# Optimization experiments

Measured on AMD Instinct MI355X. Metric: run time of the kernel, lower is better.

The kernel has to match this reference:

```python
import jax, jax.numpy as jnp
import numpy as np

H1, H2, IN, LAT = 64, 32, 2, 16

def _lstm(x, Wih, Whh, bih, bhh, H):
    # x: [B, T, I]; gate order i,f,g,o (PyTorch convention)
    B, T, _ = x.shape
    xg = jnp.einsum('bti,gi->btg', x, Wih) + bih + bhh  # [B, T, 4H]
    xg = jnp.transpose(xg, (1, 0, 2))  # [T, B, 4H]

    def step(carry, xg_t):
        h, c = carry
        gates = xg_t + h @ Whh.T
        i, f, g, o = jnp.split(gates, 4, axis=-1)
        i = jax.nn.sigmoid(i); f = jax.nn.sigmoid(f)
        g = jnp.tanh(g); o = jax.nn.sigmoid(o)
        c = f * c + i * g
        h = o * jnp.tanh(c)
        return (h, c), h

    h0 = jnp.zeros((B, H), x.dtype)
    c0 = jnp.zeros((B, H), x.dtype)
    (h_last, _), hs = jax.lax.scan(step, (h0, c0), xg)
    return jnp.transpose(hs, (1, 0, 2)), h_last  # [B,T,H], [B,H]


def setup_inputs() -> dict:
    key = jax.random.key(0)
    ks = jax.random.split(key, 12)
    s = 0.1
    return {
        'x': jax.random.normal(ks[0], (512, 4096, IN), jnp.float32),
        'Wih1': jax.random.normal(ks[1], (4 * H1, IN), jnp.float32) * s,
        'Whh1': jax.random.normal(ks[2], (4 * H1, H1), jnp.float32) * s,
        'bih1': jax.random.normal(ks[3], (4 * H1,), jnp.float32) * s,
        'bhh1': jax.random.normal(ks[4], (4 * H1,), jnp.float32) * s,
        'Wih2': jax.random.normal(ks[5], (4 * H2, H1), jnp.float32) * s,
        'Whh2': jax.random.normal(ks[6], (4 * H2, H2), jnp.float32) * s,
        'bih2': jax.random.normal(ks[7], (4 * H2,), jnp.float32) * s,
        'bhh2': jax.random.normal(ks[8], (4 * H2,), jnp.float32) * s,
        'Wfc': jax.random.normal(ks[9], (LAT, H2), jnp.float32) * s,
        'bfc': jax.random.normal(ks[10], (LAT,), jnp.float32) * s,
    }


def reference(x, Wih1, Whh1, bih1, bhh1, Wih2, Whh2, bih2, bhh2, Wfc, bfc):
    h1_seq, _ = _lstm(x, Wih1, Whh1, bih1, bhh1, H1)      # [B,T,64]
    _, h2_last = _lstm(h1_seq, Wih2, Whh2, bih2, bhh2, H2)  # [B,32] == x[:, -1, :]
    return h2_last @ Wfc.T + bfc  # [B,16]
```

## Files before the change

kernel.cpp:

```cpp
#include <hip/hip_runtime.h>


#define TT 4096
#define BB 512
#define NCH 64

typedef float    f4  __attribute__((ext_vector_type(4)));
typedef int      i4  __attribute__((ext_vector_type(4)));
typedef _Float16 h2v __attribute__((ext_vector_type(2)));
typedef _Float16 h8  __attribute__((ext_vector_type(8)));

__device__ __forceinline__ float fexp2(float x){ return __builtin_amdgcn_exp2f(x); }
__device__ __forceinline__ float frcp (float x){ return __builtin_amdgcn_rcpf(x); }
__device__ __forceinline__ float lgs  (float p){ return frcp(1.0f + fexp2(p)); }
__device__ __forceinline__ float tanh_(float x){ return 1.0f - 2.0f * frcp(1.0f + fexp2(x * 2.8853900817779268f)); }

#define BARRIER() asm volatile("s_waitcnt lgkmcnt(0)\n\ts_barrier" ::: "memory")

template<int CTRL>
__device__ __forceinline__ float qperm(float v){
  const int s = __builtin_bit_cast(int, v);
  return __builtin_bit_cast(float, __builtin_amdgcn_update_dpp(s, s, CTRL, 0xF, 0xF, true));
}
__device__ __forceinline__ h2v bch(int s){ return __builtin_bit_cast(h2v, s); }
__device__ __forceinline__ float dot8(h8 a, i4 bi, float c){
  const i4 ai = __builtin_bit_cast(i4, a);
  c = __builtin_amdgcn_fdot2(bch(ai.x), bch(bi.x), c, false);
  c = __builtin_amdgcn_fdot2(bch(ai.y), bch(bi.y), c, false);
  c = __builtin_amdgcn_fdot2(bch(ai.z), bch(bi.z), c, false);
  c = __builtin_amdgcn_fdot2(bch(ai.w), bch(bi.w), c, false);
  return c;
}
__device__ __forceinline__ float fdh(int a, int b, float c){
  return __builtin_amdgcn_fdot2(bch(a), bch(b), c, false);
}
__device__ __forceinline__ int pack16(float a, float b){
  h2v p; p.x = (_Float16)a; p.y = (_Float16)b;
  return __builtin_bit_cast(int, p);
}
__device__ __forceinline__ h8 ldh8s(const float* p, float s){
  const f4 a = ((const f4*)p)[0], b = ((const f4*)p)[1];
  h8 r;
  r[0]=(_Float16)(a.x*s); r[1]=(_Float16)(a.y*s); r[2]=(_Float16)(a.z*s); r[3]=(_Float16)(a.w*s);
  r[4]=(_Float16)(b.x*s); r[5]=(_Float16)(b.y*s); r[6]=(_Float16)(b.z*s); r[7]=(_Float16)(b.w*s);
  return r;
}

extern "C" __global__ __launch_bounds__(256, 1) void lstm_enc_kernel(
    const float* __restrict__ x,
    const float* __restrict__ Wih1, const float* __restrict__ Whh1,
    const float* __restrict__ bih1, const float* __restrict__ bhh1,
    const float* __restrict__ Wih2, const float* __restrict__ Whh2,
    const float* __restrict__ bih2, const float* __restrict__ bhh2,
    const float* __restrict__ Wfc,  const float* __restrict__ bfc,
    float* __restrict__ out)
{
    const int tid = threadIdx.x;
    const int l   = tid & 63;
    const int wv  = __builtin_amdgcn_readfirstlane(tid >> 6);
    const int be  = wv >> 1;
    const bool isL1 = ((wv & 1) == 0);
    const int bg  = blockIdx.x * 2 + be;

    __shared__ __align__(16) _Float16 ring[2][128][64];
    __shared__ __align__(16) _Float16 h2r[2][2][32];
    __shared__ int xs[2][2][64];

    const float kSs = -1.4426950408889634f;
    const float kSg = -2.8853900817779268f;

    if (isL1) {
        h8 wi[8], wf[8], wg[8], wo[8];
        const int ri = l, rf = 64 + l, rg = 128 + l, ro = 192 + l;
        #pragma unroll
        for (int j = 0; j < 8; ++j) {
            wi[j] = ldh8s(Whh1 + ri*64 + j*8, kSs);
            wf[j] = ldh8s(Whh1 + rf*64 + j*8, kSs);
            wg[j] = ldh8s(Whh1 + rg*64 + j*8, kSg);
            wo[j] = ldh8s(Whh1 + ro*64 + j*8, kSs);
        }
        const int wxi = pack16(Wih1[ri*2]*kSs, Wih1[ri*2+1]*kSs);
        const int wxf = pack16(Wih1[rf*2]*kSs, Wih1[rf*2+1]*kSs);
        const int wxg = pack16(Wih1[rg*2]*kSg, Wih1[rg*2+1]*kSg);
        const int wxo = pack16(Wih1[ro*2]*kSs, Wih1[ro*2+1]*kSs);
        const float bi_ = (bih1[ri] + bhh1[ri]) * kSs;
        const float bf_ = (bih1[rf] + bhh1[rf]) * kSs;
        const float bg_ = (bih1[rg] + bhh1[rg]) * kSg;
        const float bo_ = (bih1[ro] + bhh1[ro]) * kSs;

        if (l < 32) ((int*)&ring[be][127][0])[l] = 0;
        BARRIER();

        float cc = 0.f;
        _Float16* rw = &ring[be][0][0];
        const i4* rd = (const i4*)&ring[be][0][0];

#define L1S(PR, CR, XV) { \
    const i4* Hp = rd + (PR)*8; \
    i4 H[8]; \
    _Pragma("unroll") for (int j = 0; j < 8; ++j) H[j] = Hp[j]; \
    float ai = bi_, af = bf_, ag = bg_, ao = bo_; \
    _Pragma("unroll") for (int j = 0; j < 8; ++j) { \
        ai = dot8(wi[j], H[j], ai); af = dot8(wf[j], H[j], af); \
        ag = dot8(wg[j], H[j], ag); ao = dot8(wo[j], H[j], ao); } \
    const int xv_ = (XV); \
    ai = fdh(wxi, xv_, ai); af = fdh(wxf, xv_, af); \
    ag = fdh(wxg, xv_, ag); ao = fdh(wxo, xv_, ao); \
    const float gi = lgs(ai), gf = lgs(af), go = lgs(ao); \
    const float gg = fmaf(2.f, lgs(ag), -1.f); \
    cc = fmaf(gf, cc, gi * gg); \
    rw[(CR)*64 + l] = (_Float16)(go * tanh_(cc)); }

        #pragma unroll 1
        for (int c = 0; c <= NCH; ++c) {
            if (c < NCH) {
                const int base = (c & 1) * 64;
                const int p0 = (base ^ 64) + 63;
                const int* xc = xs[be][c & 1];
                L1S(p0, base, xc[0])
                #pragma unroll 2
                for (int s = 1; s < 64; ++s) { L1S(base + s - 1, base + s, xc[s]) }
            }
            BARRIER();
        }
#undef L1S
    } else {
        const int u = l & 31, hf = l >> 5;
        const float hff = (float)hf;
        const int rA = hf * 64 + u;
        const int rB = hf * 64 + 32 + u;
        const float kA = hf ? kSg : kSs;
        h8 wa[12], wb[12];
        #pragma unroll
        for (int j = 0; j < 8; ++j) {
            wa[j] = ldh8s(Wih2 + rA*64 + j*8, kA);
            wb[j] = ldh8s(Wih2 + rB*64 + j*8, kSs);
        }
        #pragma unroll
        for (int j = 0; j < 4; ++j) {
            wa[8+j] = ldh8s(Whh2 + rA*32 + j*8, kA);
            wb[8+j] = ldh8s(Whh2 + rB*32 + j*8, kSs);
        }
        const float ba_ = (bih2[rA] + bhh2[rA]) * kA;
        const float bb_ = (bih2[rB] + bhh2[rB]) * kSs;

        const float2* xb2 = (const float2*)(x + (size_t)bg * (TT * 2));
        {
            const float2 c0 = xb2[l];
            xs[be][0][l] = pack16(c0.x, c0.y);
        }
        float2 vxn = xb2[64 + l];
        BARRIER();

        float c2 = 0.f;
        int hp2 = 0;
        const i4* rdh = (const i4*)&ring[be][0][0];
        _Float16* q0 = &h2r[be][0][0];
        _Float16* q1 = &h2r[be][1][0];

#define L2S(S, QW) { \
    const i4* Hp = rc + (S)*8; \
    i4 H[8]; \
    _Pragma("unroll") for (int j = 0; j < 8; ++j) H[j] = Hp[j]; \
    i4 G[4]; \
    _Pragma("unroll") for (int j = 0; j < 4; ++j) { \
        G[j].x = __builtin_amdgcn_readlane(hp2, j*8+0); \
        G[j].y = __builtin_amdgcn_readlane(hp2, j*8+2); \
        G[j].z = __builtin_amdgcn_readlane(hp2, j*8+4); \
        G[j].w = __builtin_amdgcn_readlane(hp2, j*8+6); } \
    float pa = ba_, pb = bb_; \
    _Pragma("unroll") for (int j = 0; j < 8; ++j) { \
        pa = dot8(wa[j], H[j], pa); pb = dot8(wb[j], H[j], pb); } \
    _Pragma("unroll") for (int j = 0; j < 4; ++j) { \
        pa = dot8(wa[8+j], G[j], pa); pb = dot8(wb[8+j], G[j], pb); } \
    const float sa = lgs(pa); \
    const float va = fmaf(hff, sa - 1.f, sa);    \
    const float vb = lgs(pb);                    \
    const float oa = __shfl_xor(va, 32); \
    const float ob = __shfl_xor(vb, 32); \
    const float gi = hf ? oa : va, gf = hf ? ob : vb; \
    const float gg = hf ? va : oa, go = hf ? vb : ob; \
    c2 = fmaf(gf, c2, gi * gg); \
    const float h2n = go * tanh_(c2); \
    hp2 = pack16(h2n, qperm<0xB1>(h2n)); \
    if (!hf) (QW)[u] = (_Float16)h2n; }

        #pragma unroll 1
        for (int c = 0; c <= NCH; ++c) {
            if (c + 1 < NCH) xs[be][(c + 1) & 1][l] = pack16(vxn.x, vxn.y);
            if (c + 2 < NCH) vxn = xb2[(c + 2) * 64 + l];
            if (c > 0) {
                const i4* rc = rdh + ((c - 1) & 1) * 64 * 8;
                for (int s = 0; s < 64; s += 2) {
                    L2S(s,     q0)
                    L2S(s + 1, q1)
                }
            }
            BARRIER();
        }
#undef L2S

        if (l < 16) {
            float sum = bfc[l];
            const float* wr = Wfc + l * 32;
            #pragma unroll
            for (int k = 0; k < 32; ++k) sum = fmaf(wr[k], (float)h2r[be][1][k], sum);
            out[bg * 16 + l] = sum;
        }
    }
}

extern "C" void kernel_launch(void* const* d_in, const int* in_sizes, int n_in,
                              void* d_out, int out_size, void* d_ws, size_t ws_size,
                              hipStream_t stream) {
    const float* x    = (const float*)d_in[0];
    const float* Wih1 = (const float*)d_in[1];
    const float* Whh1 = (const float*)d_in[2];
    const float* bih1 = (const float*)d_in[3];
    const float* bhh1 = (const float*)d_in[4];
    const float* Wih2 = (const float*)d_in[5];
    const float* Whh2 = (const float*)d_in[6];
    const float* bih2 = (const float*)d_in[7];
    const float* bhh2 = (const float*)d_in[8];
    const float* Wfc  = (const float*)d_in[9];
    const float* bfc  = (const float*)d_in[10];

    hipLaunchKernelGGL(lstm_enc_kernel, dim3(BB / 2), dim3(256), 0, stream,
        x, Wih1, Whh1, bih1, bhh1, Wih2, Whh2, bih2, bhh2, Wfc, bfc,
        (float*)d_out);
}
```

Baseline: 1.557 ms.

## Feed x to layer-1 via readlane and double-buffer layer-2 ring reads

Layer-1 waves now load their own x chunk from global memory into a register and pass each timestep's value with readlane. This replaces the shared-memory xs buffer that the layer-2 waves used to fill, and removes the per-step LDS read of x on the layer-1 critical path. Layer-2 software-pipelines its ring reads: the h1 vector for the next step is loaded into a second register set while the current step computes, hiding LDS latency. The costs are higher register pressure and a global load issued from the latency-critical layer-1 wave.

Measured after the change: 1.484 ms (median of 3 runs). 1.05x faster.

```diff
diff --git a/kernel.cpp b/kernel.cpp
--- a/kernel.cpp
+++ b/kernel.cpp
@@ -64,7 +64,6 @@
 
     __shared__ __align__(16) _Float16 ring[2][128][64];
     __shared__ __align__(16) _Float16 h2r[2][2][32];
-    __shared__ int xs[2][2][64];
 
     const float kSs = -1.4426950408889634f;
     const float kSg = -2.8853900817779268f;
@@ -87,6 +86,11 @@
         const float bf_ = (bih1[rf] + bhh1[rf]) * kSs;
         const float bg_ = (bih1[rg] + bhh1[rg]) * kSg;
         const float bo_ = (bih1[ro] + bhh1[ro]) * kSs;
+
+        const float2* xb2 = (const float2*)(x + (size_t)bg * (TT * 2));
+        const float2 v0 = xb2[l];
+        int vxcur = pack16(v0.x, v0.y);
+        float2 vxn = xb2[64 + l];
 
         if (l < 32) ((int*)&ring[be][127][0])[l] = 0;
         BARRIER();
@@ -116,10 +120,13 @@
             if (c < NCH) {
                 const int base = (c & 1) * 64;
                 const int p0 = (base ^ 64) + 63;
-                const int* xc = xs[be][c & 1];
-                L1S(p0, base, xc[0])
+                L1S(p0, base, __builtin_amdgcn_readlane(vxcur, 0))
                 #pragma unroll 2
-                for (int s = 1; s < 64; ++s) { L1S(base + s - 1, base + s, xc[s]) }
+                for (int s = 1; s < 64; ++s) {
+                    L1S(base + s - 1, base + s, __builtin_amdgcn_readlane(vxcur, s))
+                }
+                if (c + 1 < NCH) vxcur = pack16(vxn.x, vxn.y);
+                if (c + 2 < NCH) vxn = xb2[(c + 2) * 64 + l];
             }
             BARRIER();
         }
@@ -144,12 +151,6 @@
         const float ba_ = (bih2[rA] + bhh2[rA]) * kA;
         const float bb_ = (bih2[rB] + bhh2[rB]) * kSs;
 
-        const float2* xb2 = (const float2*)(x + (size_t)bg * (TT * 2));
-        {
-            const float2 c0 = xb2[l];
-            xs[be][0][l] = pack16(c0.x, c0.y);
-        }
-        float2 vxn = xb2[64 + l];
         BARRIER();
 
         float c2 = 0.f;
@@ -158,10 +159,7 @@
         _Float16* q0 = &h2r[be][0][0];
         _Float16* q1 = &h2r[be][1][0];
 
-#define L2S(S, QW) { \
-    const i4* Hp = rc + (S)*8; \
-    i4 H[8]; \
-    _Pragma("unroll") for (int j = 0; j < 8; ++j) H[j] = Hp[j]; \
+#define L2SD(HB, QW) { \
     i4 G[4]; \
     _Pragma("unroll") for (int j = 0; j < 4; ++j) { \
         G[j].x = __builtin_amdgcn_readlane(hp2, j*8+0); \
@@ -170,7 +168,7 @@
         G[j].w = __builtin_amdgcn_readlane(hp2, j*8+6); } \
     float pa = ba_, pb = bb_; \
     _Pragma("unroll") for (int j = 0; j < 8; ++j) { \
-        pa = dot8(wa[j], H[j], pa); pb = dot8(wb[j], H[j], pb); } \
+        pa = dot8(wa[j], HB[j], pa); pb = dot8(wb[j], HB[j], pb); } \
     _Pragma("unroll") for (int j = 0; j < 4; ++j) { \
         pa = dot8(wa[8+j], G[j], pa); pb = dot8(wb[8+j], G[j], pb); } \
     const float sa = lgs(pa); \
@@ -187,18 +185,26 @@
 
         #pragma unroll 1
         for (int c = 0; c <= NCH; ++c) {
-            if (c + 1 < NCH) xs[be][(c + 1) & 1][l] = pack16(vxn.x, vxn.y);
-            if (c + 2 < NCH) vxn = xb2[(c + 2) * 64 + l];
             if (c > 0) {
                 const i4* rc = rdh + ((c - 1) & 1) * 64 * 8;
+                i4 Ha[8], Hb[8];
+                #pragma unroll
+                for (int j = 0; j < 8; ++j) Ha[j] = rc[j];
+                #pragma unroll 1
                 for (int s = 0; s < 64; s += 2) {
-                    L2S(s,     q0)
-                    L2S(s + 1, q1)
+                    const i4* rn1 = rc + (s + 1) * 8;
+                    #pragma unroll
+                    for (int j = 0; j < 8; ++j) Hb[j] = rn1[j];
+                    L2SD(Ha, q0)
+                    const i4* rn2 = rc + ((s + 2 < 64) ? (s + 2) : 0) * 8;
+                    #pragma unroll
+                    for (int j = 0; j < 8; ++j) Ha[j] = rn2[j];
+                    L2SD(Hb, q1)
                 }
             }
             BARRIER();
         }
-#undef L2S
+#undef L2SD
 
         if (l < 16) {
             float sum = bfc[l];
```

## Interleave two batch elements per wave to hide recurrent latency

Applied to the files above, without the earlier changes.

Each wavefront now processes two batch elements at once: one wave runs layer 1 for both, the other runs layer 2 for both, so a block drops from four waves to two. The two independent recurrences are interleaved in one instruction stream, giving instruction-level parallelism that hides dot/exp/LDS latency in the serial chain. The x inputs are now prefetched in registers by the layer-1 wave and broadcast with readlane, replacing the shared xs buffer. The cost is higher register pressure and half as many waves per block, which may reduce latency hiding across waves.

Result: slower. 2.852 ms (+83.3%).

```diff
diff --git a/kernel.cpp b/kernel.cpp
--- a/kernel.cpp
+++ b/kernel.cpp
@@ -46,7 +46,7 @@
   return r;
 }
 
-extern "C" __global__ __launch_bounds__(256, 1) void lstm_enc_kernel(
+extern "C" __global__ __launch_bounds__(128, 1) void lstm_enc_kernel(
     const float* __restrict__ x,
     const float* __restrict__ Wih1, const float* __restrict__ Whh1,
     const float* __restrict__ bih1, const float* __restrict__ bhh1,
@@ -58,18 +58,16 @@
     const int tid = threadIdx.x;
     const int l   = tid & 63;
     const int wv  = __builtin_amdgcn_readfirstlane(tid >> 6);
-    const int be  = wv >> 1;
-    const bool isL1 = ((wv & 1) == 0);
-    const int bg  = blockIdx.x * 2 + be;
+    const int bg0 = blockIdx.x * 2;
+    const int bg1 = bg0 + 1;
 
     __shared__ __align__(16) _Float16 ring[2][128][64];
     __shared__ __align__(16) _Float16 h2r[2][2][32];
-    __shared__ int xs[2][2][64];
 
     const float kSs = -1.4426950408889634f;
     const float kSg = -2.8853900817779268f;
 
-    if (isL1) {
+    if (wv == 0) {
         h8 wi[8], wf[8], wg[8], wo[8];
         const int ri = l, rf = 64 + l, rg = 128 + l, ro = 192 + l;
         #pragma unroll
@@ -88,42 +86,71 @@
         const float bg_ = (bih1[rg] + bhh1[rg]) * kSg;
         const float bo_ = (bih1[ro] + bhh1[ro]) * kSs;
 
-        if (l < 32) ((int*)&ring[be][127][0])[l] = 0;
+        const float2* xb0 = (const float2*)(x + (size_t)bg0 * (TT * 2));
+        const float2* xb1 = (const float2*)(x + (size_t)bg1 * (TT * 2));
+        const float2 u0 = xb0[l], u1 = xb1[l];
+        int vxc0 = pack16(u0.x, u0.y);
+        int vxc1 = pack16(u1.x, u1.y);
+        float2 vxn0 = xb0[64 + l], vxn1 = xb1[64 + l];
+
+        if (l < 32) {
+            ((int*)&ring[0][127][0])[l] = 0;
+            ((int*)&ring[1][127][0])[l] = 0;
+        }
         BARRIER();
 
-        float cc = 0.f;
-        _Float16* rw = &ring[be][0][0];
-        const i4* rd = (const i4*)&ring[be][0][0];
-
-#define L1S(PR, CR, XV) { \
-    const i4* Hp = rd + (PR)*8; \
-    i4 H[8]; \
-    _Pragma("unroll") for (int j = 0; j < 8; ++j) H[j] = Hp[j]; \
-    float ai = bi_, af = bf_, ag = bg_, ao = bo_; \
+        float cc0 = 0.f, cc1 = 0.f;
+        _Float16* rw0 = &ring[0][0][0];
+        _Float16* rw1 = &ring[1][0][0];
+        const i4* rd0 = (const i4*)&ring[0][0][0];
+        const i4* rd1 = (const i4*)&ring[1][0][0];
+
+#define L1P(PR, CR, XV0, XV1) { \
+    const i4* Hp0 = rd0 + (PR)*8; \
+    const i4* Hp1 = rd1 + (PR)*8; \
+    i4 H0[8], H1[8]; \
+    _Pragma("unroll") for (int j = 0; j < 8; ++j) H0[j] = Hp0[j]; \
+    _Pragma("unroll") for (int j = 0; j < 8; ++j) H1[j] = Hp1[j]; \
+    float a0i = bi_, a0f = bf_, a0g = bg_, a0o = bo_; \
+    float a1i = bi_, a1f = bf_, a1g = bg_, a1o = bo_; \
     _Pragma("unroll") for (int j = 0; j < 8; ++j) { \
-        ai = dot8(wi[j], H[j], ai); af = dot8(wf[j], H[j], af); \
-        ag = dot8(wg[j], H[j], ag); ao = dot8(wo[j], H[j], ao); } \
-    const int xv_ = (XV); \
-    ai = fdh(wxi, xv_, ai); af = fdh(wxf, xv_, af); \
-    ag = fdh(wxg, xv_, ag); ao = fdh(wxo, xv_, ao); \
-    const float gi = lgs(ai), gf = lgs(af), go = lgs(ao); \
-    const float gg = fmaf(2.f, lgs(ag), -1.f); \
-    cc = fmaf(gf, cc, gi * gg); \
-    rw[(CR)*64 + l] = (_Float16)(go * tanh_(cc)); }
+        a0i = dot8(wi[j], H0[j], a0i); a0f = dot8(wf[j], H0[j], a0f); \
+        a0g = dot8(wg[j], H0[j], a0g); a0o = dot8(wo[j], H0[j], a0o); \
+        a1i = dot8(wi[j], H1[j], a1i); a1f = dot8(wf[j], H1[j], a1f); \
+        a1g = dot8(wg[j], H1[j], a1g); a1o = dot8(wo[j], H1[j], a1o); } \
+    const int xv0_ = (XV0), xv1_ = (XV1); \
+    a0i = fdh(wxi, xv0_, a0i); a0f = fdh(wxf, xv0_, a0f); \
+    a0g = fdh(wxg, xv0_, a0g); a0o = fdh(wxo, xv0_, a0o); \
+    a1i = fdh(wxi, xv1_, a1i); a1f = fdh(wxf, xv1_, a1f); \
+    a1g = fdh(wxg, xv1_, a1g); a1o = fdh(wxo, xv1_, a1o); \
+    const float gi0 = lgs(a0i), gf0 = lgs(a0f), go0 = lgs(a0o); \
+    const float gg0 = fmaf(2.f, lgs(a0g), -1.f); \
+    const float gi1 = lgs(a1i), gf1 = lgs(a1f), go1 = lgs(a1o); \
+    const float gg1 = fmaf(2.f, lgs(a1g), -1.f); \
+    cc0 = fmaf(gf0, cc0, gi0 * gg0); \
+    cc1 = fmaf(gf1, cc1, gi1 * gg1); \
+    rw0[(CR)*64 + l] = (_Float16)(go0 * tanh_(cc0)); \
+    rw1[(CR)*64 + l] = (_Float16)(go1 * tanh_(cc1)); }
 
         #pragma unroll 1
         for (int c = 0; c <= NCH; ++c) {
             if (c < NCH) {
                 const int base = (c & 1) * 64;
                 const int p0 = (base ^ 64) + 63;
-                const int* xc = xs[be][c & 1];
-                L1S(p0, base, xc[0])
-                #pragma unroll 2
-                for (int s = 1; s < 64; ++s) { L1S(base + s - 1, base + s, xc[s]) }
+                L1P(p0, base, __builtin_amdgcn_readlane(vxc0, 0),
+                              __builtin_amdgcn_readlane(vxc1, 0))
+                #pragma unroll 1
+                for (int s = 1; s < 64; ++s) {
+                    L1P(base + s - 1, base + s,
+                        __builtin_amdgcn_readlane(vxc0, s),
+                        __builtin_amdgcn_readlane(vxc1, s))
+                }
+                if (c + 1 < NCH) { vxc0 = pack16(vxn0.x, vxn0.y); vxc1 = pack16(vxn1.x, vxn1.y); }
+                if (c + 2 < NCH) { vxn0 = xb0[(c + 2) * 64 + l]; vxn1 = xb1[(c + 2) * 64 + l]; }
             }
             BARRIER();
         }
-#undef L1S
+#undef L1P
     } else {
         const int u = l & 31, hf = l >> 5;
         const float hff = (float)hf;
@@ -144,68 +171,84 @@
         const float ba_ = (bih2[rA] + bhh2[rA]) * kA;
         const float bb_ = (bih2[rB] + bhh2[rB]) * kSs;
 
-        const float2* xb2 = (const float2*)(x + (size_t)bg * (TT * 2));
-        {
-            const float2 c0 = xb2[l];
-            xs[be][0][l] = pack16(c0.x, c0.y);
-        }
-        float2 vxn = xb2[64 + l];
         BARRIER();
 
-        float c2 = 0.f;
-        int hp2 = 0;
-        const i4* rdh = (const i4*)&ring[be][0][0];
-        _Float16* q0 = &h2r[be][0][0];
-        _Float16* q1 = &h2r[be][1][0];
-
-#define L2S(S, QW) { \
-    const i4* Hp = rc + (S)*8; \
-    i4 H[8]; \
-    _Pragma("unroll") for (int j = 0; j < 8; ++j) H[j] = Hp[j]; \
-    i4 G[4]; \
+        float c20 = 0.f, c21 = 0.f;
+        int hp20 = 0, hp21 = 0;
+        const i4* rdh0 = (const i4*)&ring[0][0][0];
+        const i4* rdh1 = (const i4*)&ring[1][0][0];
+        _Float16* q00 = &h2r[0][0][0];
+        _Float16* q01 = &h2r[0][1][0];
+        _Float16* q10 = &h2r[1][0][0];
+        _Float16* q11 = &h2r[1][1][0];
+
+#define L2P(S, QW0, QW1) { \
+    const i4* Hp0 = rc0 + (S)*8; \
+    const i4* Hp1 = rc1 + (S)*8; \
+    i4 H0[8], H1[8]; \
+    _Pragma("unroll") for (int j = 0; j < 8; ++j) H0[j] = Hp0[j]; \
+    _Pragma("unroll") for (int j = 0; j < 8; ++j) H1[j] = Hp1[j]; \
+    i4 G0[4], G1[4]; \
     _Pragma("unroll") for (int j = 0; j < 4; ++j) { \
-        G[j].x = __builtin_amdgcn_readlane(hp2, j*8+0); \
-        G[j].y = __builtin_amdgcn_readlane(hp2, j*8+2); \
-        G[j].z = __builtin_amdgcn_readlane(hp2, j*8+4); \
-        G[j].w = __builtin_amdgcn_readlane(hp2, j*8+6); } \
-    float pa = ba_, pb = bb_; \
+        G0[j].x = __builtin_amdgcn_readlane(hp20, j*8+0); \
+        G0[j].y = __builtin_amdgcn_readlane(hp20, j*8+2); \
+        G0[j].z = __builtin_amdgcn_readlane(hp20, j*8+4); \
+        G0[j].w = __builtin_amdgcn_readlane(hp20, j*8+6); \
+        G1[j].x = __builtin_amdgcn_readlane(hp21, j*8+0); \
+        G1[j].y = __builtin_amdgcn_readlane(hp21, j*8+2); \
+        G1[j].z = __builtin_amdgcn_readlane(hp21, j*8+4); \
+        G1[j].w = __builtin_amdgcn_readlane(hp21, j*8+6); } \
+    float pa0 = ba_, pb0 = bb_, pa1 = ba_, pb1 = bb_; \
     _Pragma("unroll") for (int j = 0; j < 8; ++j) { \
-        pa = dot8(wa[j], H[j], pa); pb = dot8(wb[j], H[j], pb); } \
+        pa0 = dot8(wa[j], H0[j], pa0); pb0 = dot8(wb[j], H0[j], pb0); \
+        pa1 = dot8(wa[j], H1[j], pa1); pb1 = dot8(wb[j], H1[j], pb1); } \
     _Pragma("unroll") for (int j = 0; j < 4; ++j) { \
-        pa = dot8(wa[8+j], G[j], pa); pb = dot8(wb[8+j], G[j], pb); } \
-    const float sa = lgs(pa); \
-    const float va = fmaf(hff, sa - 1.f, sa);    \
-    const float vb = lgs(pb);                    \
-    const float oa = __shfl_xor(va, 32); \
-    const float ob = __shfl_xor(vb, 32); \
-    const float gi = hf ? oa : va, gf = hf ? ob : vb; \
-    const float gg = hf ? va : oa, go = hf ? vb : ob; \
-    c2 = fmaf(gf, c2, gi * gg); \
-    const float h2n = go * tanh_(c2); \
-    hp2 = pack16(h2n, qperm<0xB1>(h2n)); \
-    if (!hf) (QW)[u] = (_Float16)h2n; }
+        pa0 = dot8(wa[8+j], G0[j], pa0); pb0 = dot8(wb[8+j], G0[j], pb0); \
+        pa1 = dot8(wa[8+j], G1[j], pa1); pb1 = dot8(wb[8+j], G1[j], pb1); } \
+    const float sa0 = lgs(pa0); \
+    const float va0 = fmaf(hff, sa0 - 1.f, sa0); \
+    const float vb0 = lgs(pb0); \
+    const float sa1 = lgs(pa1); \
+    const float va1 = fmaf(hff, sa1 - 1.f, sa1); \
+    const float vb1 = lgs(pb1); \
+    const float oa0 = __shfl_xor(va0, 32); \
+    const float ob0 = __shfl_xor(vb0, 32); \
+    const float oa1 = __shfl_xor(va1, 32); \
+    const float ob1 = __shfl_xor(vb1, 32); \
+    const float gi0 = hf ? oa0 : va0, gf0 = hf ? ob0 : vb0; \
+    const float gg0 = hf ? va0 : oa0, go0 = hf ? vb0 : ob0; \
+    const float gi1 = hf ? oa1 : va1, gf1 = hf ? ob1 : vb1; \
+    const float gg1 = hf ? va1 : oa1, go1 = hf ? vb1 : ob1; \
+    c20 = fmaf(gf0, c20, gi0 * gg0); \
+    c21 = fmaf(gf1, c21, gi1 * gg1); \
+    const float h2n0 = go0 * tanh_(c20); \
+    const float h2n1 = go1 * tanh_(c21); \
+    hp20 = pack16(h2n0, qperm<0xB1>(h2n0)); \
+    hp21 = pack16(h2n1, qperm<0xB1>(h2n1)); \
+    if (!hf) { (QW0)[u] = (_Float16)h2n0; (QW1)[u] = (_Float16)h2n1; } }
 
         #pragma unroll 1
         for (int c = 0; c <= NCH; ++c) {
-            if (c + 1 < NCH) xs[be][(c + 1) & 1][l] = pack16(vxn.x, vxn.y);
-            if (c + 2 < NCH) vxn = xb2[(c + 2) * 64 + l];
             if (c > 0) {
-                const i4* rc = rdh + ((c - 1) & 1) * 64 * 8;
+                const i4* rc0 = rdh0 + ((c - 1) & 1) * 64 * 8;
+                const i4* rc1 = rdh1 + ((c - 1) & 1) * 64 * 8;
+                #pragma unroll 1
                 for (int s = 0; s < 64; s += 2) {
-                    L2S(s,     q0)
-                    L2S(s + 1, q1)
+                    L2P(s,     q00, q10)
+                    L2P(s + 1, q01, q11)
                 }
             }
             BARRIER();
         }
-#undef L2S
-
-        if (l < 16) {
-            float sum = bfc[l];
-            const float* wr = Wfc + l * 32;
+#undef L2P
+
+        const int fb = l >> 5, fl = l & 31;
+        if (fl < 16) {
+            float sum = bfc[fl];
+            const float* wr = Wfc + fl * 32;
             #pragma unroll
-            for (int k = 0; k < 32; ++k) sum = fmaf(wr[k], (float)h2r[be][1][k], sum);
-            out[bg * 16 + l] = sum;
+            for (int k = 0; k < 32; ++k) sum = fmaf(wr[k], (float)h2r[fb][1][k], sum);
+            out[(bg0 + fb) * 16 + fl] = sum;
         }
     }
 }
@@ -225,7 +268,7 @@
     const float* Wfc  = (const float*)d_in[9];
     const float* bfc  = (const float*)d_in[10];
 
-    hipLaunchKernelGGL(lstm_enc_kernel, dim3(BB / 2), dim3(256), 0, stream,
+    hipLaunchKernelGGL(lstm_enc_kernel, dim3(BB / 2), dim3(128), 0, stream,
         x, Wih1, Whh1, bih1, bhh1, Wih2, Whh2, bih2, bhh2, Wfc, bfc,
         (float*)d_out);
 }
```
